# Optimization experiments

Measured on AMD Instinct MI355X. Metric: run time of the kernel, lower is better.

## Reference

```python
import jax, jax.numpy as jnp
import numpy as np

DT = 5e-05
NUM_SUBSTEPS = 100
SPRING_Y = 30000.0
DASHPOT_DAMPING = 100.0
DRAG_DAMPING = 1.0
N_VERTICES = 100000
N_SPRINGS = 1000000


def setup_inputs() -> dict:
    key = jax.random.key(0)
    k1, k2, k3, k4 = jax.random.split(key, 4)
    x = jax.random.normal(k1, (N_VERTICES, 3), dtype=jnp.float32)
    x = x.at[:, 2].add(3.0)  # start mostly above the ground plane z=0
    # spring endpoints, guaranteed distinct so rest length / norm is never 0
    idx1 = jax.random.randint(k2, (N_SPRINGS,), 0, N_VERTICES)
    off = jax.random.randint(k3, (N_SPRINGS,), 1, N_VERTICES)
    idx2 = (idx1 + off) % N_VERTICES
    springs = jnp.stack([idx1, idx2], axis=1).astype(jnp.int64)
    # rest lengths = initial spring lengths (realistic: starts near equilibrium)
    rest = jnp.linalg.norm(x[idx2] - x[idx1], axis=1).astype(jnp.float32)
    masses = jax.random.uniform(k4, (N_VERTICES,), jnp.float32, 0.5, 1.5)
    return {
        "init_vertices": x,
        "init_springs": springs,
        "init_rest_lengths": rest,
        "init_masses": masses,
    }


def reference(init_vertices, init_springs, init_rest_lengths, init_masses):
    idx1 = init_springs[:, 0]
    idx2 = init_springs[:, 1]
    masses = init_masses[:, None]                      # [V,1]
    rest = init_rest_lengths[:, None]                  # [S,1]
    gravity = jnp.array([0.0, 0.0, -9.8], dtype=init_vertices.dtype)
    drag = jnp.exp(jnp.asarray(-DT * DRAG_DAMPING, dtype=init_vertices.dtype))

    def substep(carry, _):
        x, v = carry
        dis = x[idx2] - x[idx1]                        # [S,3] gather
        length = jnp.linalg.norm(dis, axis=1, keepdims=True)
        d = dis / length                               # unit spring direction
        spring_f = SPRING_Y * (length / rest - 1.0) * d
        v_rel = jnp.sum((v[idx2] - v[idx1]) * d, axis=1, keepdims=True)
        f_pair = spring_f + DASHPOT_DAMPING * v_rel * d  # fused spring+dashpot
        forces = masses * gravity                      # [V,3]
        forces = forces.at[idx1].add(f_pair)           # scatter-add
        forces = forces.at[idx2].add(-f_pair)
        v = (v + DT * forces / masses) * drag          # explicit Euler + drag
        x = x + DT * v
        x = x.at[:, 2].set(jnp.maximum(x[:, 2], 0.0))  # ground clamp
        v = v.at[:, 2].set(jnp.where(x[:, 2] == 0.0, 0.0, v[:, 2]))
        return (x, v), None

    v0 = jnp.zeros_like(init_vertices)
    (x, v), _ = jax.lax.scan(substep, (init_vertices, v0), None, length=NUM_SUBSTEPS)
    return x
```

## Files before the change

### kernel.cpp

```cpp
#include <hip/hip_runtime.h>
#include <hip/hip_fp16.h>

#define DT 5e-5f
#define SPRING_Y 30000.0f
#define DASHPOT 100.0f
#define DRAG 0.9999500012499792f
#define NSUB 100



__device__ __forceinline__ float packv(float x, float y, float z) {
    if (fmaxf(fmaxf(fabsf(x), fabsf(y)), fabsf(z)) > 0.249f)
        return __uint_as_float(0x80000000u);
    unsigned qx = (unsigned)(x * 2048.0f + 512.5f);
    unsigned qy = (unsigned)(y * 2048.0f + 512.5f);
    unsigned qz = (unsigned)(z * 2048.0f + 512.5f);
    return __uint_as_float((qx << 20) | (qy << 10) | qz);
}

__device__ __forceinline__ float3 getvel(float w, const float4* __restrict__ V,
                                         int n) {
    unsigned uw = __float_as_uint(w);
    if (uw & 0x80000000u) {
        float4 vf = V[n];
        return make_float3(vf.x, vf.y, vf.z);
    }
    float3 v;
    v.x = (float)((int)((uw >> 20) & 1023u) - 512) * (1.0f / 2048.0f);
    v.y = (float)((int)((uw >> 10) & 1023u) - 512) * (1.0f / 2048.0f);
    v.z = (float)((int)( uw        & 1023u) - 512) * (1.0f / 2048.0f);
    return v;
}


__global__ void init_k(const float* __restrict__ x0, float4* __restrict__ G,
                       float4* __restrict__ V, int* __restrict__ deg, int nv) {
    int i = blockIdx.x * blockDim.x + threadIdx.x;
    if (i < nv) {
        G[i] = make_float4(x0[3 * i], x0[3 * i + 1], x0[3 * i + 2],
                           packv(0.f, 0.f, 0.f));
        V[i] = make_float4(0.f, 0.f, 0.f, 0.f);
        deg[i] = 0;
    }
}

__global__ void count_k(const int2* __restrict__ springs, int* __restrict__ deg,
                        int ns) {
    int s = blockIdx.x * blockDim.x + threadIdx.x;
    if (s >= ns) return;
    int2 p = springs[s];
    atomicAdd(&deg[p.x], 1);
    atomicAdd(&deg[p.y], 1);
}

__global__ void scan1_k(const int* __restrict__ deg, int* __restrict__ rowstart,
                        int* __restrict__ bsum, int nv) {
    __shared__ int sh[256];
    int t = threadIdx.x;
    int i = blockIdx.x * 256 + t;
    int v = (i < nv) ? ((deg[i] + 15) & ~15) : 0;
    sh[t] = v;
    __syncthreads();
    for (int off = 1; off < 256; off <<= 1) {
        int add = (t >= off) ? sh[t - off] : 0;
        __syncthreads();
        sh[t] += add;
        __syncthreads();
    }
    if (i < nv) rowstart[i] = sh[t] - v;
    if (t == 255) bsum[blockIdx.x] = sh[255];
}

__global__ void scan2_k(int* __restrict__ bsum, int nb) {
    __shared__ int sh[512];
    int t = threadIdx.x;
    int v = (t < nb) ? bsum[t] : 0;
    sh[t] = v;
    __syncthreads();
    for (int off = 1; off < 512; off <<= 1) {
        int add = (t >= off) ? sh[t - off] : 0;
        __syncthreads();
        sh[t] += add;
        __syncthreads();
    }
    if (t < nb) bsum[t] = sh[t] - v;
}

__global__ void scan3_k(int* __restrict__ rowstart, const int* __restrict__ bsum,
                        const int* __restrict__ deg, int* __restrict__ cursor,
                        int2* __restrict__ meta, int nv) {
    int i = blockIdx.x * blockDim.x + threadIdx.x;
    if (i < nv) {
        int r = rowstart[i] + bsum[blockIdx.x];
        rowstart[i] = r;
        cursor[i]   = r;
        meta[i]     = make_int2(r, deg[i]);
    }
}

__global__ void place_sliced_k(const int2* __restrict__ springs,
                               const float* __restrict__ rest,
                               int* __restrict__ cursor, unsigned* __restrict__ csr,
                               int ns, int nv) {
    int b = blockIdx.x;
    int slice = b & 7;
    int s = (b >> 3) * blockDim.x + threadIdx.x;
    if (s >= ns) return;

    int lo = (int)(((long long)slice * nv) >> 3);
    int hi = (int)(((long long)(slice + 1) * nv) >> 3);

    int2 p = springs[s];
    unsigned h = __half_as_ushort(__float2half(1.0f / rest[s])) & 0x7fffu;
    if (p.x >= lo && p.x < hi)
        csr[atomicAdd(&cursor[p.x], 1)] = ((unsigned)p.y << 15) | h;
    if (p.y >= lo && p.y < hi)
        csr[atomicAdd(&cursor[p.y], 1)] = ((unsigned)p.x << 15) | h;
}

__global__ void pad_k(const int2* __restrict__ meta, unsigned* __restrict__ csr,
                      int nv) {
    int v = blockIdx.x * blockDim.x + threadIdx.x;
    if (v >= nv) return;
    int2 md = meta[v];
    if (md.y > 0 && (md.y & 1)) csr[md.x + md.y] = csr[md.x];
}


__device__ __forceinline__ void accum(
        unsigned e, float4 g, const float4* __restrict__ Vin, float msk,
        const float4& ga, const float3& va,
        float& fx, float& fy, float& fz) {
    float invr = __uint_as_float(((e & 0x7fffu) << 13) + (112u << 23));
    float dx = g.x - ga.x, dy = g.y - ga.y, dz = g.z - ga.z;
    float3 vb = getvel(g.w, Vin, (int)(e >> 15));
    float len = sqrtf(dx * dx + dy * dy + dz * dz);
    float il = 1.0f / len;
    float ddx = dx * il, ddy = dy * il, ddz = dz * il;
    float vrel = (vb.x - va.x) * ddx + (vb.y - va.y) * ddy + (vb.z - va.z) * ddz;
    float coef = (SPRING_Y * (len * invr - 1.0f) + DASHPOT * vrel) * msk;
    fx += coef * ddx;
    fy += coef * ddy;
    fz += coef * ddz;
}

__global__ void __launch_bounds__(256) substep_k(
        const float4* __restrict__ Gin, float4* __restrict__ Gout,
        const float4* __restrict__ Vin, float4* __restrict__ Vout,
        const unsigned* __restrict__ csr, const int2* __restrict__ meta,
        const float* __restrict__ mass, int nv,
        float* __restrict__ out) {
    int gid = blockIdx.x * blockDim.x + threadIdx.x;
    int vid = gid >> 3;
    int sub = gid & 7;
    if (vid >= nv) return;

    int2 md = meta[vid];
    int d = md.y;
    float4 ga = Gin[vid];
    float3 va = getvel(ga.w, Vin, vid);
    int niter = (d > 2 * sub) ? ((d - 2 * sub + 15) >> 4) : 0;
    const uint2* ap = (const uint2*)(csr + md.x) + sub;

    float fx = 0.0f, fy = 0.0f, fz = 0.0f;

    for (int u = 0; u < niter; ++u) {
        uint2 q = ap[8 * u];
        float4 g0 = Gin[(int)(q.x >> 15)];
        float4 g1 = Gin[(int)(q.y >> 15)];
        accum(q.x, g0, Vin, 1.0f, ga, va, fx, fy, fz);
        float msk1 = (16 * u + 2 * sub + 1 < d) ? 1.0f : 0.0f;
        accum(q.y, g1, Vin, msk1, ga, va, fx, fy, fz);
    }

    fx += __shfl_xor(fx, 1);
    fx += __shfl_xor(fx, 2);
    fx += __shfl_xor(fx, 4);
    fy += __shfl_xor(fy, 1);
    fy += __shfl_xor(fy, 2);
    fy += __shfl_xor(fy, 4);
    fz += __shfl_xor(fz, 1);
    fz += __shfl_xor(fz, 2);
    fz += __shfl_xor(fz, 4);

    if (sub == 0) {
        float4 vf = Vin[vid];
        float m = mass[vid];
        fz += m * (-9.8f);
        float invm = 1.0f / m;

        vf.x = (vf.x + DT * fx * invm) * DRAG;
        vf.y = (vf.y + DT * fy * invm) * DRAG;
        vf.z = (vf.z + DT * fz * invm) * DRAG;

        float px = ga.x + DT * vf.x;
        float py = ga.y + DT * vf.y;
        float pz = ga.z + DT * vf.z;
        pz = fmaxf(pz, 0.0f);
        if (pz == 0.0f) vf.z = 0.0f;

        Gout[vid] = make_float4(px, py, pz, packv(vf.x, vf.y, vf.z));
        Vout[vid] = vf;

        if (out) {
            out[3 * vid + 0] = px;
            out[3 * vid + 1] = py;
            out[3 * vid + 2] = pz;
        }
    }
}

extern "C" void kernel_launch(void* const* d_in, const int* in_sizes, int n_in,
                              void* d_out, int out_size, void* d_ws, size_t ws_size,
                              hipStream_t stream) {
    const float* x0      = (const float*)d_in[0];
    const int2*  springs = (const int2*)d_in[1];
    const float* rest    = (const float*)d_in[2];
    const float* mass    = (const float*)d_in[3];

    const int ns = in_sizes[2];
    const int nv = in_sizes[3];
    const int nb = (nv + 255) / 256;

    char* ws = (char*)d_ws;
    size_t o = 0;
    float4* Ga    = (float4*)(ws + o); o += (size_t)nv * 16;
    float4* Gb    = (float4*)(ws + o); o += (size_t)nv * 16;
    float4* Va    = (float4*)(ws + o); o += (size_t)nv * 16;
    float4* Vb    = (float4*)(ws + o); o += (size_t)nv * 16;
    int* deg      = (int*)(ws + o);    o += (((size_t)nv * 4 + 15) & ~15ull);
    int* rowstart = (int*)(ws + o);    o += (((size_t)nv * 4 + 15) & ~15ull);
    int* cursor   = (int*)(ws + o);    o += (((size_t)nv * 4 + 15) & ~15ull);
    int2* meta    = (int2*)(ws + o);   o += (size_t)nv * 8;
    int* bsum     = (int*)(ws + o);    o += 512 * 4;
    o = (o + 63) & ~63ull;
    unsigned* csr = (unsigned*)(ws + o);

    dim3 blk(256);
    dim3 vgrid(nb);
    dim3 sgrid((ns + 255) / 256);
    dim3 pgrid(8 * ((ns + 255) / 256));
    dim3 subgrid(((size_t)nv * 8 + 255) / 256);

    init_k<<<vgrid, blk, 0, stream>>>(x0, Ga, Va, deg, nv);
    count_k<<<sgrid, blk, 0, stream>>>(springs, deg, ns);
    scan1_k<<<vgrid, blk, 0, stream>>>(deg, rowstart, bsum, nv);
    scan2_k<<<dim3(1), dim3(512), 0, stream>>>(bsum, nb);
    scan3_k<<<vgrid, blk, 0, stream>>>(rowstart, bsum, deg, cursor, meta, nv);
    place_sliced_k<<<pgrid, blk, 0, stream>>>(springs, rest, cursor, csr, ns, nv);
    pad_k<<<vgrid, blk, 0, stream>>>(meta, csr, nv);

    float4* Gi = Ga; float4* Go = Gb;
    float4* Vi = Va; float4* Vo = Vb;
    for (int t = 0; t < NSUB; ++t) {
        float* out = (t == NSUB - 1) ? (float*)d_out : nullptr;
        substep_k<<<subgrid, blk, 0, stream>>>(Gi, Go, Vi, Vo, csr, meta,
                                               mass, nv, out);
        float4* tg = Gi; Gi = Go; Go = tg;
        float4* tv = Vi; Vi = Vo; Vo = tv;
    }
}
```

Before: 1.967 ms.

## Replace per-substep launches with persistent kernel and grid-wide flag barrier

Swaps the 100 separate substep kernel launches for one persistent kernel sized at two blocks per CU. The blocks walk the vertices with a grid stride and sync between substeps through per-block done flags using release stores and polling loads. The aim is to remove per-launch overhead and the tail of each launch. In exchange there is a spin-barrier cost every substep and less parallelism per substep, since only 2*CU blocks of 32 vertices each are resident. There is also a deadlock or race risk if not all blocks are co-resident, and the spin loop bails out after a bounded count.

```diff
diff --git a/kernel.cpp b/kernel.cpp
--- a/kernel.cpp
+++ b/kernel.cpp
@@ -71,9 +71,10 @@
     if (t == 255) bsum[blockIdx.x] = sh[255];
 }
 
-__global__ void scan2_k(int* __restrict__ bsum, int nb) {
+__global__ void scan2_k(int* __restrict__ bsum, int nb, int* __restrict__ done) {
     __shared__ int sh[512];
     int t = threadIdx.x;
+    done[t] = 0;
     int v = (t < nb) ? bsum[t] : 0;
     sh[t] = v;
     __syncthreads();
@@ -144,6 +145,104 @@
     fz += coef * ddz;
 }
 
+__device__ __forceinline__ void do_vertex(
+        int vid, int sub,
+        const float4* __restrict__ Gin, float4* __restrict__ Gout,
+        const float4* __restrict__ Vin, float4* __restrict__ Vout,
+        const unsigned* __restrict__ csr, const int2* __restrict__ meta,
+        const float* __restrict__ mass, float* __restrict__ out) {
+    int2 md = meta[vid];
+    int d = md.y;
+    float4 ga = Gin[vid];
+    float3 va = getvel(ga.w, Vin, vid);
+    int niter = (d > 2 * sub) ? ((d - 2 * sub + 15) >> 4) : 0;
+    const uint2* ap = (const uint2*)(csr + md.x) + sub;
+
+    float fx = 0.0f, fy = 0.0f, fz = 0.0f;
+    for (int u = 0; u < niter; ++u) {
+        uint2 q = ap[8 * u];
+        float4 g0 = Gin[(int)(q.x >> 15)];
+        float4 g1 = Gin[(int)(q.y >> 15)];
+        accum(q.x, g0, Vin, 1.0f, ga, va, fx, fy, fz);
+        float msk1 = (16 * u + 2 * sub + 1 < d) ? 1.0f : 0.0f;
+        accum(q.y, g1, Vin, msk1, ga, va, fx, fy, fz);
+    }
+
+    fx += __shfl_xor(fx, 1); fx += __shfl_xor(fx, 2); fx += __shfl_xor(fx, 4);
+    fy += __shfl_xor(fy, 1); fy += __shfl_xor(fy, 2); fy += __shfl_xor(fy, 4);
+    fz += __shfl_xor(fz, 1); fz += __shfl_xor(fz, 2); fz += __shfl_xor(fz, 4);
+
+    if (sub == 0) {
+        float4 vf = Vin[vid];
+        float m = mass[vid];
+        fz += m * (-9.8f);
+        float invm = 1.0f / m;
+
+        vf.x = (vf.x + DT * fx * invm) * DRAG;
+        vf.y = (vf.y + DT * fy * invm) * DRAG;
+        vf.z = (vf.z + DT * fz * invm) * DRAG;
+
+        float px = ga.x + DT * vf.x;
+        float py = ga.y + DT * vf.y;
+        float pz = ga.z + DT * vf.z;
+        pz = fmaxf(pz, 0.0f);
+        if (pz == 0.0f) vf.z = 0.0f;
+
+        Gout[vid] = make_float4(px, py, pz, packv(vf.x, vf.y, vf.z));
+        Vout[vid] = vf;
+
+        if (out) {
+            out[3 * vid + 0] = px;
+            out[3 * vid + 1] = py;
+            out[3 * vid + 2] = pz;
+        }
+    }
+}
+
+
+__global__ void __launch_bounds__(256, 2) persist_k(
+        float4* Ga, float4* Gb, float4* Va, float4* Vb,
+        const unsigned* __restrict__ csr, const int2* __restrict__ meta,
+        const float* __restrict__ mass, int nv, int pb,
+        int* __restrict__ done, float* __restrict__ out) {
+    int bid = blockIdx.x;
+    int tid = threadIdx.x;
+    int sub = tid & 7;
+    int g0  = bid * 32 + (tid >> 3);
+    int gstride = pb * 32;
+
+    for (int t = 0; t < NSUB; ++t) {
+        const float4* Gin = (t & 1) ? Gb : Ga;
+        float4* Gout      = (t & 1) ? Ga : Gb;
+        const float4* Vin = (t & 1) ? Vb : Va;
+        float4* Vout      = (t & 1) ? Va : Vb;
+        float* o = (t == NSUB - 1) ? out : nullptr;
+
+        for (int vid = g0; vid < nv; vid += gstride)
+            do_vertex(vid, sub, Gin, Gout, Vin, Vout, csr, meta, mass, o);
+
+        if (t + 1 < NSUB) {
+            __syncthreads();
+            if (tid == 0) {
+                __threadfence();
+                __hip_atomic_store(&done[bid], t + 1, __ATOMIC_RELEASE,
+                                   __HIP_MEMORY_SCOPE_AGENT);
+            }
+            for (int j = tid; j < pb; j += 256) {
+                int spin = 0;
+                while (__hip_atomic_load(&done[j], __ATOMIC_RELAXED,
+                                         __HIP_MEMORY_SCOPE_AGENT) < t + 1) {
+                    __builtin_amdgcn_s_sleep(2);
+                    if (++spin > (1 << 22)) break;
+                }
+            }
+            __threadfence();
+            __syncthreads();
+        }
+    }
+}
+
+
 __global__ void __launch_bounds__(256) substep_k(
         const float4* __restrict__ Gin, float4* __restrict__ Gout,
         const float4* __restrict__ Vin, float4* __restrict__ Vout,
@@ -154,60 +253,7 @@
     int vid = gid >> 3;
     int sub = gid & 7;
     if (vid >= nv) return;
-
-    int2 md = meta[vid];
-    int d = md.y;
-    float4 ga = Gin[vid];
-    float3 va = getvel(ga.w, Vin, vid);
-    int niter = (d > 2 * sub) ? ((d - 2 * sub + 15) >> 4) : 0;
-    const uint2* ap = (const uint2*)(csr + md.x) + sub;
-
-    float fx = 0.0f, fy = 0.0f, fz = 0.0f;
-
-    for (int u = 0; u < niter; ++u) {
-        uint2 q = ap[8 * u];
-        float4 g0 = Gin[(int)(q.x >> 15)];
-        float4 g1 = Gin[(int)(q.y >> 15)];
-        accum(q.x, g0, Vin, 1.0f, ga, va, fx, fy, fz);
-        float msk1 = (16 * u + 2 * sub + 1 < d) ? 1.0f : 0.0f;
-        accum(q.y, g1, Vin, msk1, ga, va, fx, fy, fz);
-    }
-
-    fx += __shfl_xor(fx, 1);
-    fx += __shfl_xor(fx, 2);
-    fx += __shfl_xor(fx, 4);
-    fy += __shfl_xor(fy, 1);
-    fy += __shfl_xor(fy, 2);
-    fy += __shfl_xor(fy, 4);
-    fz += __shfl_xor(fz, 1);
-    fz += __shfl_xor(fz, 2);
-    fz += __shfl_xor(fz, 4);
-
-    if (sub == 0) {
-        float4 vf = Vin[vid];
-        float m = mass[vid];
-        fz += m * (-9.8f);
-        float invm = 1.0f / m;
-
-        vf.x = (vf.x + DT * fx * invm) * DRAG;
-        vf.y = (vf.y + DT * fy * invm) * DRAG;
-        vf.z = (vf.z + DT * fz * invm) * DRAG;
-
-        float px = ga.x + DT * vf.x;
-        float py = ga.y + DT * vf.y;
-        float pz = ga.z + DT * vf.z;
-        pz = fmaxf(pz, 0.0f);
-        if (pz == 0.0f) vf.z = 0.0f;
-
-        Gout[vid] = make_float4(px, py, pz, packv(vf.x, vf.y, vf.z));
-        Vout[vid] = vf;
-
-        if (out) {
-            out[3 * vid + 0] = px;
-            out[3 * vid + 1] = py;
-            out[3 * vid + 2] = pz;
-        }
-    }
+    do_vertex(vid, sub, Gin, Gout, Vin, Vout, csr, meta, mass, out);
 }
 
 extern "C" void kernel_launch(void* const* d_in, const int* in_sizes, int n_in,
@@ -233,6 +279,7 @@
     int* cursor   = (int*)(ws + o);    o += (((size_t)nv * 4 + 15) & ~15ull);
     int2* meta    = (int2*)(ws + o);   o += (size_t)nv * 8;
     int* bsum     = (int*)(ws + o);    o += 512 * 4;
+    int* done     = (int*)(ws + o);    o += 512 * 4;
     o = (o + 63) & ~63ull;
     unsigned* csr = (unsigned*)(ws + o);
 
@@ -245,18 +292,30 @@
     init_k<<<vgrid, blk, 0, stream>>>(x0, Ga, Va, deg, nv);
     count_k<<<sgrid, blk, 0, stream>>>(springs, deg, ns);
     scan1_k<<<vgrid, blk, 0, stream>>>(deg, rowstart, bsum, nv);
-    scan2_k<<<dim3(1), dim3(512), 0, stream>>>(bsum, nb);
+    scan2_k<<<dim3(1), dim3(512), 0, stream>>>(bsum, nb, done);
     scan3_k<<<vgrid, blk, 0, stream>>>(rowstart, bsum, deg, cursor, meta, nv);
     place_sliced_k<<<pgrid, blk, 0, stream>>>(springs, rest, cursor, csr, ns, nv);
     pad_k<<<vgrid, blk, 0, stream>>>(meta, csr, nv);
 
-    float4* Gi = Ga; float4* Go = Gb;
-    float4* Vi = Va; float4* Vo = Vb;
-    for (int t = 0; t < NSUB; ++t) {
-        float* out = (t == NSUB - 1) ? (float*)d_out : nullptr;
-        substep_k<<<subgrid, blk, 0, stream>>>(Gi, Go, Vi, Vo, csr, meta,
-                                               mass, nv, out);
-        float4* tg = Gi; Gi = Go; Go = tg;
-        float4* tv = Vi; Vi = Vo; Vo = tv;
-    }
-}
+    int dev = 0, ncu = 0, maxb = 0;
+    hipGetDevice(&dev);
+    hipDeviceGetAttribute(&ncu, hipDeviceAttributeMultiprocessorCount, dev);
+    hipOccupancyMaxActiveBlocksPerMultiprocessor(&maxb, persist_k, 256, 0);
+
+    if (maxb >= 2 && ncu > 0 && 2 * ncu <= 512) {
+        int pb = 2 * ncu;
+        persist_k<<<dim3(pb), blk, 0, stream>>>(Ga, Gb, Va, Vb, csr, meta,
+                                                mass, nv, pb, done,
+                                                (float*)d_out);
+    } else {
+        float4* Gi = Ga; float4* Go = Gb;
+        float4* Vi = Va; float4* Vo = Vb;
+        for (int t = 0; t < NSUB; ++t) {
+            float* out = (t == NSUB - 1) ? (float*)d_out : nullptr;
+            substep_k<<<subgrid, blk, 0, stream>>>(Gi, Go, Vi, Vo, csr, meta,
+                                                   mass, nv, out);
+            float4* tg = Gi; Gi = Go; Go = tg;
+            float4* tv = Vi; Vi = Vo; Vo = tv;
+        }
+    }
+}
```

After: 7.842 ms. 299% more time.
